# Optimization experiments

Measured on AMD Instinct MI355X. Metric: run time of the kernel, lower is better.

The kernel has to match this reference:

```python
import jax, jax.numpy as jnp
import numpy as np

B, S, HID = 2, 2048, 2048
NH, NKV, HD = 32, 8, 64
ROPE_THETA = 10000.0
SCALE = HD ** -0.5


def _rope_cos_sin(seq_len, head_dim, theta):
    inv_freq = 1.0 / (theta ** (jnp.arange(0, head_dim, 2, dtype=jnp.float32) / head_dim))
    pos = jnp.arange(seq_len, dtype=jnp.float32)
    freqs = jnp.outer(pos, inv_freq)              # [S, HD/2]
    emb = jnp.concatenate([freqs, freqs], axis=-1)  # [S, HD]
    return jnp.cos(emb), jnp.sin(emb)


def _rotate_half(x):
    x1, x2 = jnp.split(x, 2, axis=-1)
    return jnp.concatenate([-x2, x1], axis=-1)


def setup_inputs() -> dict:
    key = jax.random.key(0)
    ks = jax.random.split(key, 8)
    s = 0.02
    return {
        "hidden_states": jax.random.normal(ks[0], (B, S, HID), jnp.float32),
        "q_w": jax.random.normal(ks[1], (NH * HD, HID), jnp.float32) * s,
        "q_b": jax.random.normal(ks[2], (NH * HD,), jnp.float32) * s,
        "k_w": jax.random.normal(ks[3], (NKV * HD, HID), jnp.float32) * s,
        "k_b": jax.random.normal(ks[4], (NKV * HD,), jnp.float32) * s,
        "v_w": jax.random.normal(ks[5], (NKV * HD, HID), jnp.float32) * s,
        "v_b": jax.random.normal(ks[6], (NKV * HD,), jnp.float32) * s,
        "o_w": jax.random.normal(ks[7], (HID, NH * HD), jnp.float32) * s,
    }


def reference(hidden_states, q_w, q_b, k_w, k_b, v_w, v_b, o_w):
    bsz, q_len, _ = hidden_states.shape
    # QKV projections (nn.Linear: x @ W^T + b)
    q = hidden_states @ q_w.T + q_b   # [B, S, NH*HD]
    k = hidden_states @ k_w.T + k_b   # [B, S, NKV*HD]
    v = hidden_states @ v_w.T + v_b
    # reshape to [B, H, S, D]
    q = q.reshape(bsz, q_len, NH, HD).transpose(0, 2, 1, 3)
    k = k.reshape(bsz, q_len, NKV, HD).transpose(0, 2, 1, 3)
    v = v.reshape(bsz, q_len, NKV, HD).transpose(0, 2, 1, 3)
    # RoPE
    cos, sin = _rope_cos_sin(q_len, HD, ROPE_THETA)  # [S, HD]
    cos = cos[None, None]; sin = sin[None, None]
    q = q * cos + _rotate_half(q) * sin
    k = k * cos + _rotate_half(k) * sin
    # GQA: expand kv heads to match query heads
    groups = NH // NKV
    k = jnp.repeat(k, groups, axis=1)  # [B, NH, S, D]
    v = jnp.repeat(v, groups, axis=1)
    # scaled dot-product attention with causal mask
    scores = jnp.einsum('bhqd,bhkd->bhqk', q, k) * SCALE
    causal = jnp.tril(jnp.ones((q_len, q_len), dtype=bool))
    scores = jnp.where(causal[None, None], scores, jnp.finfo(scores.dtype).min)
    probs = jax.nn.softmax(scores, axis=-1)
    out = jnp.einsum('bhqk,bhkd->bhqd', probs, v)  # [B, NH, S, D]
    out = out.transpose(0, 2, 1, 3).reshape(bsz, q_len, NH * HD)
    return out @ o_w.T  # [B, S, HID]
```

## Files before the change

### kernel.cpp

```cpp
#include <hip/hip_runtime.h>
#include <stdint.h>
#include <stddef.h>

typedef __attribute__((ext_vector_type(8))) short s16x8;
typedef __attribute__((ext_vector_type(4))) short s16x4;
typedef __attribute__((ext_vector_type(4))) float f32x4;
typedef __attribute__((ext_vector_type(2))) unsigned int u32x2;

#define S_LEN 2048
#define HID 2048
#define QKV_N 3072
#define NHEAD 32
#define NKVH 8

__device__ __forceinline__ unsigned short f2bf(float f) {
  union { float f; unsigned u; } a; a.f = f;
  unsigned u = a.u;
  u += 0x7fffu + ((u >> 16) & 1u);
  return (unsigned short)(u >> 16);
}
__device__ __forceinline__ float bf2f(unsigned short h) {
  union { unsigned u; float f; } a; a.u = ((unsigned)h) << 16;
  return a.f;
}
__device__ __forceinline__ unsigned cvt_pk_bf16(float a, float b) {
  unsigned r;
  asm("v_cvt_pk_bf16_f32 %0, %1, %2" : "=v"(r) : "v"(a), "v"(b));
  return r;
}
__device__ __forceinline__ void gl_lds16(const unsigned short* g, short* l) {
  __builtin_amdgcn_global_load_lds(
      (const __attribute__((address_space(1))) unsigned int*)g,
      (__attribute__((address_space(3))) unsigned int*)l, 16, 0, 0);
}

__global__ void k_convert(const float* __restrict__ x, const float* __restrict__ wq,
                          const float* __restrict__ wk, const float* __restrict__ wv,
                          const float* __restrict__ wo, unsigned short* __restrict__ dst) {
  const unsigned n4 = 18874368u / 4u;
  for (unsigned i = blockIdx.x * blockDim.x + threadIdx.x; i < n4;
       i += gridDim.x * blockDim.x) {
    unsigned e = i * 4u;
    const float* src; unsigned off;
    if (e < 8388608u)       { src = x;  off = e; }
    else if (e < 12582912u) { src = wq; off = e - 8388608u; }
    else if (e < 13631488u) { src = wk; off = e - 12582912u; }
    else if (e < 14680064u) { src = wv; off = e - 13631488u; }
    else                    { src = wo; off = e - 14680064u; }
    f32x4 v = *(const f32x4*)(src + off);
    s16x4 o;
    o[0] = (short)f2bf(v[0]); o[1] = (short)f2bf(v[1]);
    o[2] = (short)f2bf(v[2]); o[3] = (short)f2bf(v[3]);
    *(s16x4*)(dst + e) = o;
  }
}

__global__ void k_rope_table(float* __restrict__ cost, float* __restrict__ sint) {
  int idx = blockIdx.x * 256 + threadIdx.x;
  int i = idx & 31, s = idx >> 5;
  float inv = powf(10000.0f, -(float)(2 * i) / 64.0f);
  float ang = (float)s * inv;
  cost[idx] = cosf(ang);
  sint[idx] = sinf(ang);
}

template <int MODE>
__global__ __launch_bounds__(256) void k_gemm(
    const unsigned short* __restrict__ A,
    const unsigned short* __restrict__ W0, const unsigned short* __restrict__ W1,
    const unsigned short* __restrict__ W2,
    const float* __restrict__ b0, const float* __restrict__ b1, const float* __restrict__ b2,
    const float* __restrict__ ct, const float* __restrict__ st,
    unsigned short* __restrict__ Cb, float* __restrict__ Cf) {
  __shared__ short lA[128 * 32];
  __shared__ short lB[128 * 32];
  const int K = 2048;
  int tid = threadIdx.x;
  int wave = tid >> 6, lane = tid & 63;
  int l15 = lane & 15, lg = lane >> 4;
  int tn = blockIdx.x, tm = blockIdx.y;
  const unsigned short* W; const float* bias = nullptr; int col0;
  if constexpr (MODE == 0) {
    if (tn < 16)      { W = W0; bias = b0; col0 = tn * 128; }
    else if (tn < 20) { W = W1; bias = b1; col0 = (tn - 16) * 128; }
    else              { W = W2; bias = b2; col0 = (tn - 20) * 128; }
  } else { W = W0; col0 = tn * 128; }
  int m0 = tm * 128;
  int wm = wave >> 1, wn = wave & 1;

  const unsigned short* gA0 = A + (size_t)(m0 + (tid >> 2)) * K + (tid & 3) * 8;
  const unsigned short* gA1 = gA0 + (size_t)64 * K;
  const unsigned short* gB0 = W + (size_t)(col0 + (tid >> 2)) * K + (tid & 3) * 8;
  const unsigned short* gB1 = gB0 + (size_t)64 * K;
  short* sA0 = &lA[wave * 512];
  short* sA1 = &lA[2048 + wave * 512];
  short* sB0 = &lB[wave * 512];
  short* sB1 = &lB[2048 + wave * 512];

  f32x4 acc[4][4];
#pragma unroll
  for (int m = 0; m < 4; ++m)
#pragma unroll
    for (int n = 0; n < 4; ++n) acc[m][n] = (f32x4){0.f, 0.f, 0.f, 0.f};

  for (int kt = 0; kt < K; kt += 32) {
    __syncthreads();
    gl_lds16(gA0 + kt, sA0);
    gl_lds16(gA1 + kt, sA1);
    gl_lds16(gB0 + kt, sB0);
    gl_lds16(gB1 + kt, sB1);
    asm volatile("s_waitcnt vmcnt(0)" ::: "memory");
    __syncthreads();
    s16x8 af[4], bfr[4];
    const short* pa = &lA[(wm * 64 + l15) * 32 + lg * 8];
    const short* pb = &lB[(wn * 64 + l15) * 32 + lg * 8];
#pragma unroll
    for (int m = 0; m < 4; ++m) af[m] = *(const s16x8*)(pa + m * 512);
#pragma unroll
    for (int n = 0; n < 4; ++n) bfr[n] = *(const s16x8*)(pb + n * 512);
#pragma unroll
    for (int m = 0; m < 4; ++m)
#pragma unroll
      for (int n = 0; n < 4; ++n)
        acc[m][n] = __builtin_amdgcn_mfma_f32_16x16x32_bf16(af[m], bfr[n], acc[m][n], 0, 0, 0);
  }

  if constexpr (MODE == 0) {
    bool rope = (tn < 20);
#pragma unroll
    for (int n = 0; n < 2; ++n) {
      int lcol = col0 + wn * 64 + n * 16 + l15;
      int gcol = tn * 128 + wn * 64 + n * 16 + l15;
      float blo = bias[lcol], bhi = bias[lcol + 32];
      int i = n * 16 + l15;
#pragma unroll
      for (int m = 0; m < 4; ++m) {
        int row = m0 + wm * 64 + m * 16 + lg * 4;
#pragma unroll
        for (int r = 0; r < 4; ++r) {
          float xl = acc[m][n][r] + blo;
          float xh = acc[m][n + 2][r] + bhi;
          if (rope) {
            int s = (row + r) & (S_LEN - 1);
            float c = ct[s * 32 + i], sn = st[s * 32 + i];
            float nl = xl * c - xh * sn;
            xh = xh * c + xl * sn;
            xl = nl;
          }
          Cb[(size_t)(row + r) * QKV_N + gcol] = f2bf(xl);
          Cb[(size_t)(row + r) * QKV_N + gcol + 32] = f2bf(xh);
        }
      }
    }
  } else {
#pragma unroll
    for (int n = 0; n < 4; ++n) {
      int gcol = tn * 128 + wn * 64 + n * 16 + l15;
#pragma unroll
      for (int m = 0; m < 4; ++m) {
        int row = m0 + wm * 64 + m * 16 + lg * 4;
#pragma unroll
        for (int r = 0; r < 4; ++r)
          Cf[(size_t)(row + r) * HID + gcol] = acc[m][n][r];
      }
    }
  }
}

__global__ void k_vtrans(const unsigned short* __restrict__ qkv, unsigned short* __restrict__ vt) {
  __shared__ unsigned short t[64][80];
  int ts = blockIdx.x & 63, td = blockIdx.x >> 6;
  int tid = threadIdx.x;
#pragma unroll
  for (int L = 0; L < 2; ++L) {
    int c = L * 256 + tid;
    int row = c >> 3, ch = c & 7;
    const unsigned short* src = qkv + (size_t)(ts * 64 + row) * QKV_N + 2560 + td * 64 + ch * 8;
    s16x8 v = *(const s16x8*)src;
    int cs = (ch * 8) ^ ((row >> 3) << 3);
    *(s16x8*)&t[row][cs] = v;
  }
  __syncthreads();
  int b = (ts * 64) >> 11;
  int s0 = (ts * 64) & (S_LEN - 1);
#pragma unroll
  for (int L = 0; L < 2; ++L) {
    int c = L * 256 + tid;
    int d = c >> 3, sc = c & 7;
    s16x8 o;
#pragma unroll
    for (int j = 0; j < 8; ++j) o[j] = (short)t[sc * 8 + j][d ^ (sc << 3)];
    unsigned short* dst = vt + ((size_t)((b * 8 + td) * 64 + d)) * 2048 + s0 + sc * 8;
    *(s16x8*)dst = o;
  }
}

__global__ __launch_bounds__(512, 4) void k_attn(const unsigned short* __restrict__ qkv,
                                                 const unsigned short* __restrict__ vt,
                                                 unsigned short* __restrict__ aout) {
  __shared__ unsigned short lK[2][4096];
  __shared__ unsigned short lV[2][4096];
  __shared__ unsigned short pl[8][2048];
  int wave = threadIdx.x >> 6, lane = threadIdx.x & 63;
  int l15 = lane & 15, lg = lane >> 4;
  int bi = blockIdx.x;
  int ip = bi >> 4;
  int b  = (bi >> 3) & 1;
  int hg = bi & 7;
  int wgrp = wave >> 2;
  int wh = wave & 3;
  int h = hg * 4 + wh;
  int t = wgrp ? ip : (63 - ip);
  int q0 = t * 32;
  int kbend = t >> 1;
  int kbmaxB = (63 - ip) >> 1;

  const unsigned short* qb_ = qkv + (size_t)(b * S_LEN) * QKV_N + h * 64;
  const unsigned short* kbase = qkv + (size_t)(b * S_LEN) * QKV_N + 2048 + hg * 64;
  const unsigned short* vbase = vt + (size_t)((b * NKVH + hg) * 64) * 2048;
  unsigned short* pw = &pl[wave][0];
  int sw = (l15 & 7) << 3;

  int srow = wave * 8 + (lane >> 3);
  int ssw = 8 * ((lane & 7) ^ ((lane >> 3) & 7));
  const unsigned short* gk0 = kbase + (size_t)srow * QKV_N + ssw;
  const unsigned short* gv0 = vbase + (size_t)srow * 2048 + ssw;
  short* lkd0 = (short*)&lK[0][wave * 512]; short* lkd1 = (short*)&lK[1][wave * 512];
  short* lvd0 = (short*)&lV[0][wave * 512]; short* lvd1 = (short*)&lV[1][wave * 512];

  s16x8 aq[2][2];
#pragma unroll
  for (int m = 0; m < 2; ++m)
#pragma unroll
    for (int ks = 0; ks < 2; ++ks)
      aq[m][ks] = *(const s16x8*)(qb_ + (size_t)(q0 + m * 16 + l15) * QKV_N + ks * 32 + lg * 8);

  f32x4 acc[2][4];
  float mrow[2], lrow[2];
#pragma unroll
  for (int m = 0; m < 2; ++m) {
#pragma unroll
    for (int dt = 0; dt < 4; ++dt) acc[m][dt] = (f32x4){0.f, 0.f, 0.f, 0.f};
    mrow[m] = -3.0e38f; lrow[m] = 0.f;
  }

  const float CSC = 0.125f * 1.44269504f;

  gl_lds16(gk0, lkd0);
  gl_lds16(gv0, lvd0);
  asm volatile("s_waitcnt vmcnt(0)" ::: "memory");
  __syncthreads();

  for (int kb = 0; kb <= kbmaxB; ++kb) {
    const unsigned short* lk = &lK[kb & 1][0];
    const unsigned short* lv = &lV[kb & 1][0];
    if (kb < kbmaxB) {
      size_t go = (size_t)(kb + 1) * 64;
      if ((kb & 1) == 0) { gl_lds16(gk0 + go * QKV_N, lkd1); gl_lds16(gv0 + go, lvd1); }
      else               { gl_lds16(gk0 + go * QKV_N, lkd0); gl_lds16(gv0 + go, lvd0); }
    }
    if (kb <= kbend) {
      bool need_mask = (kb == kbend);
#pragma unroll
      for (int m = 0; m < 2; ++m) {
        f32x4 z[4];
        __builtin_amdgcn_s_setprio(1);
#pragma unroll
        for (int nt = 0; nt < 4; ++nt) {
          s16x8 k0 = *(const s16x8*)(lk + (nt * 16 + l15) * 64 + ((lg * 8) ^ sw));
          s16x8 k1 = *(const s16x8*)(lk + (nt * 16 + l15) * 64 + ((32 + lg * 8) ^ sw));
          f32x4 zz = (f32x4){0.f, 0.f, 0.f, 0.f};
          zz = __builtin_amdgcn_mfma_f32_16x16x32_bf16(k0, aq[m][0], zz, 0, 0, 0);
          zz = __builtin_amdgcn_mfma_f32_16x16x32_bf16(k1, aq[m][1], zz, 0, 0, 0);
          z[nt] = zz;
        }
        __builtin_amdgcn_s_setprio(0);
        float s[16];
        int q = q0 + m * 16 + l15;
#pragma unroll
        for (int nt = 0; nt < 4; ++nt)
#pragma unroll
          for (int r = 0; r < 4; ++r) {
            float v = z[nt][r] * CSC;
            if (need_mask) {
              int k = kb * 64 + nt * 16 + lg * 4 + r;
              if (k > q) v = -1.0e30f;
            }
            s[nt * 4 + r] = v;
          }
        float m01 = fmaxf(s[0], s[1]), m23 = fmaxf(s[2], s[3]);
        float m45 = fmaxf(s[4], s[5]), m67 = fmaxf(s[6], s[7]);
        float m89 = fmaxf(s[8], s[9]), mab = fmaxf(s[10], s[11]);
        float mcd = fmaxf(s[12], s[13]), mef = fmaxf(s[14], s[15]);
        float mx = fmaxf(fmaxf(fmaxf(m01, m23), fmaxf(m45, m67)),
                         fmaxf(fmaxf(m89, mab), fmaxf(mcd, mef)));
        mx = fmaxf(mx, __shfl_xor(mx, 16));
        mx = fmaxf(mx, __shfl_xor(mx, 32));
        if (!__all(mx <= mrow[m] + 8.0f)) {
          float nm = fmaxf(mrow[m], mx);
          float corr = __builtin_amdgcn_exp2f(mrow[m] - nm);
          mrow[m] = nm;
          lrow[m] *= corr;
#pragma unroll
          for (int r = 0; r < 4; ++r) {
            float cr = __shfl(corr, lg * 4 + r);
#pragma unroll
            for (int dt = 0; dt < 4; ++dt) acc[m][dt][r] *= cr;
          }
        }
        float nm = mrow[m];
        float rs = 0.f;
#pragma unroll
        for (int nt = 0; nt < 4; ++nt) {
          float p0 = __builtin_amdgcn_exp2f(s[nt * 4 + 0] - nm);
          float p1 = __builtin_amdgcn_exp2f(s[nt * 4 + 1] - nm);
          float p2 = __builtin_amdgcn_exp2f(s[nt * 4 + 2] - nm);
          float p3 = __builtin_amdgcn_exp2f(s[nt * 4 + 3] - nm);
          rs += (p0 + p1) + (p2 + p3);
          u32x2 w;
          w[0] = cvt_pk_bf16(p0, p1);
          w[1] = cvt_pk_bf16(p2, p3);
          *(u32x2*)(pw + (m * 16 + l15) * 64 + ((nt * 16 + lg * 4) ^ sw)) = w;
        }
        rs += __shfl_xor(rs, 16);
        rs += __shfl_xor(rs, 32);
        lrow[m] += rs;
      }
      s16x8 pa[2][2];
#pragma unroll
      for (int m = 0; m < 2; ++m)
#pragma unroll
        for (int ks = 0; ks < 2; ++ks)
          pa[m][ks] = *(const s16x8*)(pw + (m * 16 + l15) * 64 + ((ks * 32 + lg * 8) ^ sw));
      __builtin_amdgcn_s_setprio(1);
#pragma unroll
      for (int dt = 0; dt < 4; ++dt) {
        s16x8 v0 = *(const s16x8*)(lv + (dt * 16 + l15) * 64 + ((lg * 8) ^ sw));
        s16x8 v1 = *(const s16x8*)(lv + (dt * 16 + l15) * 64 + ((32 + lg * 8) ^ sw));
#pragma unroll
        for (int m = 0; m < 2; ++m) {
          acc[m][dt] = __builtin_amdgcn_mfma_f32_16x16x32_bf16(pa[m][0], v0, acc[m][dt], 0, 0, 0);
          acc[m][dt] = __builtin_amdgcn_mfma_f32_16x16x32_bf16(pa[m][1], v1, acc[m][dt], 0, 0, 0);
        }
      }
      __builtin_amdgcn_s_setprio(0);
    }
    asm volatile("s_waitcnt vmcnt(0)" ::: "memory");
    __syncthreads();
  }

  unsigned short* ob = aout + (size_t)(b * S_LEN) * HID + h * 64;
#pragma unroll
  for (int m = 0; m < 2; ++m)
#pragma unroll
    for (int r = 0; r < 4; ++r) {
      float lr = __shfl(lrow[m], lg * 4 + r);
      float inv = 1.0f / lr;
#pragma unroll
      for (int dt = 0; dt < 4; ++dt)
        ob[(size_t)(q0 + m * 16 + lg * 4 + r) * HID + dt * 16 + l15] = f2bf(acc[m][dt][r] * inv);
    }
}

extern "C" void kernel_launch(void* const* d_in, const int* in_sizes, int n_in,
                              void* d_out, int out_size, void* d_ws, size_t ws_size,
                              hipStream_t stream) {
  const float* x  = (const float*)d_in[0];
  const float* qw = (const float*)d_in[1];
  const float* qb = (const float*)d_in[2];
  const float* kw = (const float*)d_in[3];
  const float* kbias = (const float*)d_in[4];
  const float* vw = (const float*)d_in[5];
  const float* vbias = (const float*)d_in[6];
  const float* ow = (const float*)d_in[7];

  unsigned short* Xb  = (unsigned short*)d_ws;
  unsigned short* Wqb = Xb + 8388608;
  unsigned short* Wkb = Wqb + 4194304;
  unsigned short* Wvb = Wkb + 1048576;
  unsigned short* Wob = Wvb + 1048576;
  unsigned short* QKV = Wob + 4194304;
  unsigned short* VT  = QKV + 12582912;
  unsigned short* AO  = VT + 2097152;
  float* COS = (float*)(AO + 8388608);
  float* SIN = COS + 65536;

  k_convert<<<1024, 256, 0, stream>>>(x, qw, kw, vw, ow, Xb);
  k_rope_table<<<256, 256, 0, stream>>>(COS, SIN);
  k_gemm<0><<<dim3(24, 32), 256, 0, stream>>>(Xb, Wqb, Wkb, Wvb, qb, kbias, vbias,
                                              COS, SIN, QKV, nullptr);
  k_vtrans<<<512, 256, 0, stream>>>(QKV, VT);
  k_attn<<<512, 512, 0, stream>>>(QKV, VT, AO);
  k_gemm<1><<<dim3(16, 32), 256, 0, stream>>>(AO, Wob, nullptr, nullptr,
                                              nullptr, nullptr, nullptr, nullptr, nullptr,
                                              nullptr, (float*)d_out);
}
```

Baseline: 208.6 us.

## Double-buffer GEMM LDS loads, swizzle tile order, fold softmax scale into Q

The projection GEMM now double-buffers its LDS tiles, issuing the next K-slice's global-to-LDS loads before the current slice's MFMAs, and raises wave priority around the MFMA block. Workgroup IDs are remapped in groups of eight, presumably to improve L2 reuse. The softmax scale is folded into Q in the GEMM epilogue, which removes a multiply per score in attention. The attention P scratch buffer is halved by reusing one 16-row slot per m, which lowers LDS use. The GEMM's LDS footprint doubles, and the extra bf16 rounding of the pre-scaled Q may change numerics slightly.

```diff
diff --git a/kernel.cpp b/kernel.cpp
--- a/kernel.cpp
+++ b/kernel.cpp
@@ -18,10 +18,6 @@
   unsigned u = a.u;
   u += 0x7fffu + ((u >> 16) & 1u);
   return (unsigned short)(u >> 16);
-}
-__device__ __forceinline__ float bf2f(unsigned short h) {
-  union { unsigned u; float f; } a; a.u = ((unsigned)h) << 16;
-  return a.f;
 }
 __device__ __forceinline__ unsigned cvt_pk_bf16(float a, float b) {
   unsigned r;
@@ -72,13 +68,17 @@
     const float* __restrict__ b0, const float* __restrict__ b1, const float* __restrict__ b2,
     const float* __restrict__ ct, const float* __restrict__ st,
     unsigned short* __restrict__ Cb, float* __restrict__ Cf) {
-  __shared__ short lA[128 * 32];
-  __shared__ short lB[128 * 32];
+  __shared__ short lA[2][4096];
+  __shared__ short lB[2][4096];
   const int K = 2048;
   int tid = threadIdx.x;
   int wave = tid >> 6, lane = tid & 63;
   int l15 = lane & 15, lg = lane >> 4;
-  int tn = blockIdx.x, tm = blockIdx.y;
+  int nwg = gridDim.x * gridDim.y;
+  int f = blockIdx.y * gridDim.x + blockIdx.x;
+  f = (f & 7) * (nwg >> 3) + (f >> 3);
+  int tn = f % gridDim.x, tm = f / gridDim.x;
+
   const unsigned short* W; const float* bias = nullptr; int col0;
   if constexpr (MODE == 0) {
     if (tn < 16)      { W = W0; bias = b0; col0 = tn * 128; }
@@ -92,10 +92,6 @@
   const unsigned short* gA1 = gA0 + (size_t)64 * K;
   const unsigned short* gB0 = W + (size_t)(col0 + (tid >> 2)) * K + (tid & 3) * 8;
   const unsigned short* gB1 = gB0 + (size_t)64 * K;
-  short* sA0 = &lA[wave * 512];
-  short* sA1 = &lA[2048 + wave * 512];
-  short* sB0 = &lB[wave * 512];
-  short* sB1 = &lB[2048 + wave * 512];
 
   f32x4 acc[4][4];
 #pragma unroll
@@ -103,30 +99,44 @@
 #pragma unroll
     for (int n = 0; n < 4; ++n) acc[m][n] = (f32x4){0.f, 0.f, 0.f, 0.f};
 
-  for (int kt = 0; kt < K; kt += 32) {
-    __syncthreads();
-    gl_lds16(gA0 + kt, sA0);
-    gl_lds16(gA1 + kt, sA1);
-    gl_lds16(gB0 + kt, sB0);
-    gl_lds16(gB1 + kt, sB1);
-    asm volatile("s_waitcnt vmcnt(0)" ::: "memory");
-    __syncthreads();
+  gl_lds16(gA0, &lA[0][wave * 512]);
+  gl_lds16(gA1, &lA[0][2048 + wave * 512]);
+  gl_lds16(gB0, &lB[0][wave * 512]);
+  gl_lds16(gB1, &lB[0][2048 + wave * 512]);
+  asm volatile("s_waitcnt vmcnt(0)" ::: "memory");
+  __syncthreads();
+
+  for (int kt = 0; kt < 64; ++kt) {
+    int cur = kt & 1;
+    if (kt < 63) {
+      int nxt = cur ^ 1;
+      int off = (kt + 1) * 32;
+      gl_lds16(gA0 + off, &lA[nxt][wave * 512]);
+      gl_lds16(gA1 + off, &lA[nxt][2048 + wave * 512]);
+      gl_lds16(gB0 + off, &lB[nxt][wave * 512]);
+      gl_lds16(gB1 + off, &lB[nxt][2048 + wave * 512]);
+    }
     s16x8 af[4], bfr[4];
-    const short* pa = &lA[(wm * 64 + l15) * 32 + lg * 8];
-    const short* pb = &lB[(wn * 64 + l15) * 32 + lg * 8];
+    const short* pa = &lA[cur][(wm * 64 + l15) * 32 + lg * 8];
+    const short* pb = &lB[cur][(wn * 64 + l15) * 32 + lg * 8];
 #pragma unroll
     for (int m = 0; m < 4; ++m) af[m] = *(const s16x8*)(pa + m * 512);
 #pragma unroll
     for (int n = 0; n < 4; ++n) bfr[n] = *(const s16x8*)(pb + n * 512);
+    __builtin_amdgcn_s_setprio(1);
 #pragma unroll
     for (int m = 0; m < 4; ++m)
 #pragma unroll
       for (int n = 0; n < 4; ++n)
         acc[m][n] = __builtin_amdgcn_mfma_f32_16x16x32_bf16(af[m], bfr[n], acc[m][n], 0, 0, 0);
+    __builtin_amdgcn_s_setprio(0);
+    __syncthreads();
   }
 
   if constexpr (MODE == 0) {
+    const float CSC = 0.125f * 1.44269504f;
     bool rope = (tn < 20);
+    bool isq = (tn < 16);
 #pragma unroll
     for (int n = 0; n < 2; ++n) {
       int lcol = col0 + wn * 64 + n * 16 + l15;
@@ -146,6 +156,7 @@
             float nl = xl * c - xh * sn;
             xh = xh * c + xl * sn;
             xl = nl;
+            if (isq) { xl *= CSC; xh *= CSC; }
           }
           Cb[(size_t)(row + r) * QKV_N + gcol] = f2bf(xl);
           Cb[(size_t)(row + r) * QKV_N + gcol + 32] = f2bf(xh);
@@ -200,7 +211,7 @@
                                                  unsigned short* __restrict__ aout) {
   __shared__ unsigned short lK[2][4096];
   __shared__ unsigned short lV[2][4096];
-  __shared__ unsigned short pl[8][2048];
+  __shared__ unsigned short pl[8][1024];
   int wave = threadIdx.x >> 6, lane = threadIdx.x & 63;
   int l15 = lane & 15, lg = lane >> 4;
   int bi = blockIdx.x;
@@ -244,8 +255,6 @@
     mrow[m] = -3.0e38f; lrow[m] = 0.f;
   }
 
-  const float CSC = 0.125f * 1.44269504f;
-
   gl_lds16(gk0, lkd0);
   gl_lds16(gv0, lvd0);
   asm volatile("s_waitcnt vmcnt(0)" ::: "memory");
@@ -261,6 +270,7 @@
     }
     if (kb <= kbend) {
       bool need_mask = (kb == kbend);
+      s16x8 pa[2][2];
 #pragma unroll
       for (int m = 0; m < 2; ++m) {
         f32x4 z[4];
@@ -281,7 +291,7 @@
         for (int nt = 0; nt < 4; ++nt)
 #pragma unroll
           for (int r = 0; r < 4; ++r) {
-            float v = z[nt][r] * CSC;
+            float v = z[nt][r];
             if (need_mask) {
               int k = kb * 64 + nt * 16 + lg * 4 + r;
               if (k > q) v = -1.0e30f;
@@ -320,18 +330,14 @@
           u32x2 w;
           w[0] = cvt_pk_bf16(p0, p1);
           w[1] = cvt_pk_bf16(p2, p3);
-          *(u32x2*)(pw + (m * 16 + l15) * 64 + ((nt * 16 + lg * 4) ^ sw)) = w;
+          *(u32x2*)(pw + l15 * 64 + ((nt * 16 + lg * 4) ^ sw)) = w;
         }
         rs += __shfl_xor(rs, 16);
         rs += __shfl_xor(rs, 32);
         lrow[m] += rs;
+        pa[m][0] = *(const s16x8*)(pw + l15 * 64 + ((lg * 8) ^ sw));
+        pa[m][1] = *(const s16x8*)(pw + l15 * 64 + ((32 + lg * 8) ^ sw));
       }
-      s16x8 pa[2][2];
-#pragma unroll
-      for (int m = 0; m < 2; ++m)
-#pragma unroll
-        for (int ks = 0; ks < 2; ++ks)
-          pa[m][ks] = *(const s16x8*)(pw + (m * 16 + l15) * 64 + ((ks * 32 + lg * 8) ^ sw));
       __builtin_amdgcn_s_setprio(1);
 #pragma unroll
       for (int dt = 0; dt < 4; ++dt) {
```

Result: slower. 218.2 us (+4.6%).
